# Kernel tuning notes

Hardware: AMD Instinct MI355X
Metric: run time of the kernel (lower is better)

Reference implementation:

```python
import jax, jax.numpy as jnp
import numpy as np
from jax.scipy.special import gammaln

PRIOR = 0.25      # downsample_rate -> Binomial prior on boundary frequency
TEMP = 1.0        # gumbel (RelaxedBernoulli) temperature
THRESHOLD = 0.5   # hard-boundary threshold

B, L, D = 8, 2048, 1024


def setup_inputs() -> dict:
    key = jax.random.key(0)
    k_x, k_u, k_w1, k_w2, k_ng = jax.random.split(key, 5)
    x = jax.random.normal(k_x, (B, L, D), dtype=jnp.float32)
    noise = jax.random.uniform(k_u, (B, L), dtype=jnp.float32)
    W1 = jax.random.normal(k_w1, (D, D), dtype=jnp.float32) / np.sqrt(D)
    b1 = jnp.zeros((D,), dtype=jnp.float32)
    W2 = jax.random.normal(k_w2, (D, 1), dtype=jnp.float32) / np.sqrt(D)
    b2 = jnp.zeros((1,), dtype=jnp.float32)
    null_group = jax.random.normal(k_ng, (1, 1, D), dtype=jnp.float32)
    return {"x": x, "noise": noise, "W1": W1, "b1": b1, "W2": W2, "b2": b2,
            "null_group": null_group}


def _common(boundaries, n_segments, upsample):
    # boundaries: [B, L] -> soft group-offset tensor foo: [B, L, S]
    hh1 = jnp.cumsum(boundaries, axis=1)
    if not upsample:
        hh1 = hh1 - boundaries
    s = jnp.arange(n_segments, dtype=boundaries.dtype)
    return s[None, None, :] - hh1[:, :, None]


def _final(foo, upsample):
    # indicator of token-l belonging to segment-s, normalized (mean-pool / gather)
    lel = jnp.where(foo != 0, 0.0, 1.0 - foo)
    axis = 2 if upsample else 1
    return lel / (jnp.sum(lel, axis=axis, keepdims=True) + 1e-9)


def reference(x, noise, W1, b1, W2, b2, null_group):
    Bn, Ln, Dn = x.shape
    S_max = Ln  # static upper bound on segment count (padded; extra segs = zeros)

    # --- boundary predictor (gumbel / RelaxedBernoulli rsample, temp=1) ---
    logits = (jax.nn.relu(x @ W1 + b1) @ W2 + b2)[..., 0]            # [B, L]
    u = jnp.clip(noise, 1e-6, 1.0 - 1e-6)
    soft = jax.nn.sigmoid((logits + jnp.log(u) - jnp.log1p(-u)) / TEMP)
    hard_val = (soft > THRESHOLD).astype(soft.dtype)
    hard = jax.lax.stop_gradient(hard_val - soft) + soft             # straight-through

    # --- downsample: mean-pool each variable-length segment ---
    bar_d = _final(_common(hard, S_max, False), False)               # [B, L, S]
    pooled = jnp.einsum('bld,bls->bsd', x, bar_d)                    # [B, S, D]
    shortened = jnp.concatenate(
        [jnp.broadcast_to(null_group, (Bn, 1, Dn)), pooled], axis=1)  # [B, S+1, D]

    # --- upsample: token l reads segment cumsum(hard)[l] (null group = 0) ---
    bar_u = _final(_common(hard, S_max + 1, True), True)             # [B, L, S+1]
    upsampled = jnp.einsum('bsd,bls->bld', shortened, bar_u)         # [B, L, D]

    # --- consistency loss: -log Binomial(L, prior).pmf(#boundaries) / L ---
    k = jnp.sum(hard, axis=-1)                                       # [B]
    Lf = jnp.asarray(Ln, soft.dtype)
    logp = (gammaln(Lf + 1.0) - gammaln(k + 1.0) - gammaln(Lf - k + 1.0)
            + k * jnp.log(PRIOR) + (Lf - k) * jnp.log1p(-PRIOR))
    loss = -jnp.mean(logp) / Ln

    return shortened, upsampled, loss
```

## Files before the change

kernel.cpp:

```cpp
#include <hip/hip_runtime.h>
#include <math.h>

#define Bq 8
#define Lq 2048
#define Dq 1024
#define Mq (Bq*Lq)
#define Sq 2048
#define SP1 2049
#define FLAG_CAP 1024
#define KSLICES 8
#define MARGIN 0.06f

typedef __attribute__((ext_vector_type(8))) short short8;
typedef __attribute__((ext_vector_type(4))) float f32x4;

static __device__ __forceinline__ ushort f2bf(float f) {
  union { float f; uint32_t u; } v; v.f = f;
  uint32_t u = v.u;
  return (ushort)((u + 0x7FFF + ((u >> 16) & 1)) >> 16);
}

static __device__ __forceinline__ void gload_lds16(const void* gsrc, void* lds) {
  __builtin_amdgcn_global_load_lds(
      (const __attribute__((address_space(1))) uint32_t*)(uintptr_t)gsrc,
      (__attribute__((address_space(3))) uint32_t*)(uint32_t)(uintptr_t)lds,
      16, 0, 0);
}

__global__ void init_logits(float* __restrict__ logits, const float* __restrict__ b2,
                            int* __restrict__ count) {
  int i = blockIdx.x * 256 + threadIdx.x;
  if (i < Mq) logits[i] = b2[0];
  if (i == 0) *count = 0;
}

__global__ void convert_x(const float* __restrict__ x, ushort* __restrict__ xb) {
  int i = blockIdx.x * 256 + threadIdx.x;
  float4 v = ((const float4*)x)[i];
  ushort4 o;
  o.x = f2bf(v.x); o.y = f2bf(v.y); o.z = f2bf(v.z); o.w = f2bf(v.w);
  ((ushort4*)xb)[i] = o;
}

__global__ void convert_w1t(const float* __restrict__ W1, ushort* __restrict__ Wt) {
  __shared__ ushort sh[32][33];
  const int tx = threadIdx.x & 31, ty = threadIdx.x >> 5;
  const int k0 = blockIdx.x * 32, n0 = blockIdx.y * 32;
  #pragma unroll
  for (int r = 0; r < 32; r += 8)
    sh[ty + r][tx] = f2bf(W1[(size_t)(k0 + ty + r) * Dq + n0 + tx]);
  __syncthreads();
  #pragma unroll
  for (int r = 0; r < 32; r += 8)
    Wt[(size_t)(n0 + ty + r) * Dq + k0 + tx] = sh[tx][ty + r];
}

__global__ __launch_bounds__(256) void mfma_gemm(
    const ushort* __restrict__ Xb,
    const ushort* __restrict__ Wt,
    const float* __restrict__ b1, const float* __restrict__ W2,
    float* __restrict__ logits)
{
  __shared__ ushort Al[128 * 32];
  __shared__ ushort Bl[128 * 32];
  __shared__ float red[128];
  const int tid = threadIdx.x;
  const int w = tid >> 6, lane = tid & 63;
  const int m0 = blockIdx.x * 128, n0 = blockIdx.y * 128;
  const int wr = w >> 1, wc = w & 1;
  const int lr = lane & 15, lq = lane >> 4;

  f32x4 acc[4][4] = {};
  if (tid < 128) red[tid] = 0.f;

  for (int kt = 0; kt < Dq; kt += 32) {
    #pragma unroll
    for (int s = 0; s < 2; ++s) {
      int rbase = s * 64 + w * 16;
      const ushort* srcA = Xb + (size_t)(m0 + rbase + (lane >> 2)) * Dq + kt + (lane & 3) * 8;
      gload_lds16(srcA, &Al[rbase * 32]);
      const ushort* srcB = Wt + (size_t)(n0 + rbase + (lane >> 2)) * Dq + kt + (lane & 3) * 8;
      gload_lds16(srcB, &Bl[rbase * 32]);
    }
    __syncthreads();
    short8 a[4], b[4];
    #pragma unroll
    for (int m = 0; m < 4; ++m)
      a[m] = *(const short8*)&Al[(wr * 64 + m * 16 + lr) * 32 + lq * 8];
    #pragma unroll
    for (int n = 0; n < 4; ++n)
      b[n] = *(const short8*)&Bl[(wc * 64 + n * 16 + lr) * 32 + lq * 8];
    #pragma unroll
    for (int m = 0; m < 4; ++m)
      #pragma unroll
      for (int n = 0; n < 4; ++n)
        acc[m][n] = __builtin_amdgcn_mfma_f32_16x16x32_bf16(a[m], b[n], acc[m][n], 0, 0, 0);
    __syncthreads();
  }

  float q[4][4];
  #pragma unroll
  for (int m = 0; m < 4; ++m)
    #pragma unroll
    for (int r = 0; r < 4; ++r) q[m][r] = 0.f;
  #pragma unroll
  for (int n = 0; n < 4; ++n) {
    int col = n0 + wc * 64 + n * 16 + lr;
    float bb = b1[col];
    float ww = W2[col];
    #pragma unroll
    for (int m = 0; m < 4; ++m)
      #pragma unroll
      for (int r = 0; r < 4; ++r) {
        float v = acc[m][n][r] + bb;
        v = v > 0.f ? v : 0.f;
        q[m][r] = fmaf(v, ww, q[m][r]);
      }
  }
  #pragma unroll
  for (int m = 0; m < 4; ++m)
    #pragma unroll
    for (int r = 0; r < 4; ++r) {
      float s = q[m][r];
      s += __shfl_xor(s, 1); s += __shfl_xor(s, 2);
      s += __shfl_xor(s, 4); s += __shfl_xor(s, 8);
      if (lr == 0) atomicAdd(&red[wr * 64 + m * 16 + lq * 4 + r], s);
    }
  __syncthreads();
  if (tid < 128) atomicAdd(&logits[m0 + tid], red[tid]);
}

__global__ void flag_kernel(const float* __restrict__ logits, const float* __restrict__ noise,
                            int* __restrict__ count, int* __restrict__ list) {
  int i = blockIdx.x * 256 + threadIdx.x;
  float u = noise[i];
  u = fminf(fmaxf(u, 1e-6f), 0.999999f);
  float z = (logits[i] + logf(u)) - log1pf(-u);
  if (fabsf(z) < MARGIN) {
    int id = atomicAdd(count, 1);
    if (id < FLAG_CAP) list[id] = i;
  }
}

__global__ __launch_bounds__(256) void fix_part1(
    const float* __restrict__ x, const float* __restrict__ W1,
    const int* __restrict__ count, const int* __restrict__ list,
    float* __restrict__ hbuf)
{
  __shared__ float Asl[32][33];
  __shared__ float Bsl[32][128];
  int cnt = *count; if (cnt > FLAG_CAP) cnt = FLAG_CAP;
  if (cnt <= 0) return;
  int tiles_m = (cnt + 31) >> 5;
  int total = tiles_m * 8 * KSLICES;
  const int tid = threadIdx.x;
  const int tx = tid & 31, ty = tid >> 5;
  for (int t = blockIdx.x; t < total; t += gridDim.x) {
    int m0 = (t / (8 * KSLICES)) * 32;
    int n0 = ((t / KSLICES) & 7) * 128;
    int kbase = (t % KSLICES) * (Dq / KSLICES);
    float C[4][4] = {};
    for (int kc = 0; kc < Dq / KSLICES; kc += 32) {
      int k0 = kbase + kc;
      __syncthreads();
      {
        int mr = tid >> 3, kf = tid & 7;
        int fidx = m0 + mr; if (fidx >= cnt) fidx = cnt - 1;
        int tok = list[fidx];
        float4 va = *(const float4*)(x + (size_t)tok * Dq + k0 + kf * 4);
        Asl[kf*4+0][mr] = va.x; Asl[kf*4+1][mr] = va.y;
        Asl[kf*4+2][mr] = va.z; Asl[kf*4+3][mr] = va.w;
      }
      #pragma unroll
      for (int s = 0; s < 4; ++s) {
        int slot = tid + s * 256;
        int kb = slot >> 5, nf = slot & 31;
        *(float4*)(&Bsl[kb][nf*4]) =
            *(const float4*)(W1 + (size_t)(k0 + kb) * Dq + n0 + nf * 4);
      }
      __syncthreads();
      #pragma unroll
      for (int k = 0; k < 32; ++k) {
        float a[4], b[4];
        #pragma unroll
        for (int i = 0; i < 4; ++i) a[i] = Asl[k][ty*4+i];
        #pragma unroll
        for (int j = 0; j < 4; ++j) b[j] = Bsl[k][tx + 32*j];
        #pragma unroll
        for (int i = 0; i < 4; ++i)
          #pragma unroll
          for (int j = 0; j < 4; ++j)
            C[i][j] = fmaf(a[i], b[j], C[i][j]);
      }
    }
    int ks = t % KSLICES;
    #pragma unroll
    for (int i = 0; i < 4; ++i) {
      int f = m0 + ty*4 + i;
      float* dst = hbuf + ((size_t)ks * FLAG_CAP + f) * Dq + n0 + tx;
      #pragma unroll
      for (int j = 0; j < 4; ++j) dst[32*j] = C[i][j];
    }
    __syncthreads();
  }
}

__global__ __launch_bounds__(256) void fix_part2(
    const float* __restrict__ hbuf, const float* __restrict__ b1,
    const float* __restrict__ W2, const float* __restrict__ b2,
    const int* __restrict__ count, const int* __restrict__ list,
    float* __restrict__ logits)
{
  __shared__ float rs[4];
  int cnt = *count; if (cnt > FLAG_CAP) cnt = FLAG_CAP;
  const int tid = threadIdx.x;
  const int lane = tid & 63, w = tid >> 6;
  float b2v = b2[0];
  for (int f = blockIdx.x; f < cnt; f += gridDim.x) {
    int n = tid * 4;
    float4 h = {0.f, 0.f, 0.f, 0.f};
    #pragma unroll
    for (int ks = 0; ks < KSLICES; ++ks) {
      float4 pv = *(const float4*)(hbuf + ((size_t)ks * FLAG_CAP + f) * Dq + n);
      h.x += pv.x; h.y += pv.y; h.z += pv.z; h.w += pv.w;
    }
    float4 bb = *(const float4*)(b1 + n);
    float4 ww = *(const float4*)(W2 + n);
    float p = 0.f;
    float v;
    v = h.x + bb.x; v = v > 0.f ? v : 0.f; p = fmaf(v, ww.x, p);
    v = h.y + bb.y; v = v > 0.f ? v : 0.f; p = fmaf(v, ww.y, p);
    v = h.z + bb.z; v = v > 0.f ? v : 0.f; p = fmaf(v, ww.z, p);
    v = h.w + bb.w; v = v > 0.f ? v : 0.f; p = fmaf(v, ww.w, p);
    #pragma unroll
    for (int off = 32; off > 0; off >>= 1) p += __shfl_xor(p, off);
    if (lane == 0) rs[w] = p;
    __syncthreads();
    if (tid == 0) logits[list[f]] = b2v + rs[0] + rs[1] + rs[2] + rs[3];
    __syncthreads();
  }
}

__global__ __launch_bounds__(256) void boundary_scan(
    const float* __restrict__ logits, const float* __restrict__ noise,
    int* __restrict__ segup, int* __restrict__ starts, int* __restrict__ ends,
    int* __restrict__ nsegs, int* __restrict__ kb)
{
  const int b = blockIdx.x;
  const int t = threadIdx.x;
  __shared__ unsigned char sh_hard[Lq];
  __shared__ int wsum[4];
  const int l0 = t * 8;
  int h[8];
  int localsum = 0;
  #pragma unroll
  for (int j = 0; j < 8; ++j) {
    int l = l0 + j;
    float u = noise[b * Lq + l];
    u = fminf(fmaxf(u, 1e-6f), 0.999999f);
    float z = (logits[b * Lq + l] + logf(u)) - log1pf(-u);
    int hd = (z > 0.f) ? 1 : 0;
    h[j] = hd;
    sh_hard[l] = (unsigned char)hd;
    localsum += hd;
  }
  int lane = t & 63, w = t >> 6;
  int v = localsum;
  #pragma unroll
  for (int off = 1; off < 64; off <<= 1) {
    int n = __shfl_up(v, off);
    if (lane >= off) v += n;
  }
  if (lane == 63) wsum[w] = v;
  __syncthreads();
  int wpre = 0;
  for (int i = 0; i < w; ++i) wpre += wsum[i];
  int run = wpre + (v - localsum);
  #pragma unroll
  for (int j = 0; j < 8; ++j) {
    int l = l0 + j;
    run += h[j];
    segup[b * Lq + l] = run;
    int sd = run - h[j];
    int hp = (l == 0) ? 1 : (int)sh_hard[l - 1];
    if (hp) starts[b * Sq + sd] = l;
    if (h[j] || l == Lq - 1) ends[b * Sq + sd] = l + 1;
    if (l == Lq - 1) { nsegs[b] = sd + 1; kb[b] = run; }
  }
}

__global__ __launch_bounds__(256) void pool_kernel(
    const float* __restrict__ x, const float* __restrict__ null_group,
    const int* __restrict__ starts, const int* __restrict__ ends,
    const int* __restrict__ nsegs, float* __restrict__ outS)
{
  const int so = blockIdx.x;
  const int b  = blockIdx.y;
  const int d4 = threadIdx.x;
  float4* dst = (float4*)(outS + ((size_t)b * SP1 + so) * Dq) + d4;
  if (so == 0) { *dst = ((const float4*)null_group)[d4]; return; }
  int s = so - 1;
  if (s >= nsegs[b]) { float4 z; z.x = z.y = z.z = z.w = 0.f; *dst = z; return; }
  int st = starts[b * Sq + s], en = ends[b * Sq + s];
  float4 acc; acc.x = acc.y = acc.z = acc.w = 0.f;
  for (int l = st; l < en; ++l) {
    float4 vv = ((const float4*)(x + ((size_t)b * Lq + l) * Dq))[d4];
    acc.x += vv.x; acc.y += vv.y; acc.z += vv.z; acc.w += vv.w;
  }
  float inv = 1.f / (float)(en - st);
  acc.x *= inv; acc.y *= inv; acc.z *= inv; acc.w *= inv;
  *dst = acc;
}

__global__ __launch_bounds__(256) void upsample_kernel(
    const float* __restrict__ outS, const int* __restrict__ segup,
    float* __restrict__ outU)
{
  const int l = blockIdx.x, b = blockIdx.y;
  const int d4 = threadIdx.x;
  int sg = segup[b * Lq + l];
  ((float4*)(outU + ((size_t)b * Lq + l) * Dq))[d4] =
      ((const float4*)(outS + ((size_t)b * SP1 + sg) * Dq))[d4];
}

__global__ void loss_kernel(const int* __restrict__ kb, float* __restrict__ out)
{
  int t = threadIdx.x;
  float lp = 0.f;
  if (t < Bq) {
    float k  = (float)kb[t];
    float Lf = (float)Lq;
    lp = lgammaf(Lf + 1.f) - lgammaf(k + 1.f) - lgammaf(Lf - k + 1.f)
       + k * logf(0.25f) + (Lf - k) * log1pf(-0.25f);
  }
  #pragma unroll
  for (int off = 32; off > 0; off >>= 1) lp += __shfl_down(lp, off);
  if (t == 0) out[0] = -(lp / (float)Bq) / (float)Lq;
}

extern "C" void kernel_launch(void* const* d_in, const int* in_sizes, int n_in,
                              void* d_out, int out_size, void* d_ws, size_t ws_size,
                              hipStream_t stream) {
  const float* x     = (const float*)d_in[0];
  const float* noise = (const float*)d_in[1];
  const float* W1    = (const float*)d_in[2];
  const float* b1    = (const float*)d_in[3];
  const float* W2    = (const float*)d_in[4];
  const float* b2    = (const float*)d_in[5];
  const float* ng    = (const float*)d_in[6];

  float* outS = (float*)d_out;
  float* outU = outS + (size_t)Bq * SP1 * Dq;
  float* outL = outU + (size_t)Bq * Lq * Dq;

  ushort* xb   = (ushort*)outU;
  ushort* wt   = (ushort*)((char*)outU + (size_t)33554432);
  float*  hbuf = outS;

  char* ws = (char*)d_ws;
  float* logits = (float*)(ws);
  int*   segup  = (int*)(ws + 65536);
  int*   starts = (int*)(ws + 131072);
  int*   ends   = (int*)(ws + 196608);
  int*   nsegs  = (int*)(ws + 262144);
  int*   kb     = (int*)(ws + 262400);
  int*   count  = (int*)(ws + 262656);
  int*   list   = (int*)(ws + 262912);

  init_logits<<<Mq / 256, 256, 0, stream>>>(logits, b2, count);
  convert_x<<<(Mq * Dq / 4) / 256, 256, 0, stream>>>(x, xb);
  convert_w1t<<<dim3(32, 32), 256, 0, stream>>>(W1, wt);
  mfma_gemm<<<dim3(Mq / 128, Dq / 128), 256, 0, stream>>>(xb, wt, b1, W2, logits);
  flag_kernel<<<Mq / 256, 256, 0, stream>>>(logits, noise, count, list);
  fix_part1<<<2048, 256, 0, stream>>>(x, W1, count, list, hbuf);
  fix_part2<<<1024, 256, 0, stream>>>(hbuf, b1, W2, b2, count, list, logits);
  boundary_scan<<<Bq, 256, 0, stream>>>(logits, noise, segup, starts, ends, nsegs, kb);
  pool_kernel<<<dim3(SP1, Bq), 256, 0, stream>>>(x, ng, starts, ends, nsegs, outS);
  upsample_kernel<<<dim3(Lq, Bq), 256, 0, stream>>>(outS, segup, outU);
  loss_kernel<<<1, 64, 0, stream>>>(kb, outL);
}
```

Measured before the change: 311.9 us.

## Fuse conversion kernels and merge pooling with upsample scatter

Merges logits init, x conversion and W1 transpose-conversion into a single launch. Swaps the GEMM grid axes so consecutive blocks share an M row tile and read different W columns. Replaces the separate upsample kernel with a scatter inside the pool kernel: each segment block writes its pooled value directly to the token rows of the upsample output. This uses per-segment boundary positions computed in the scan, so the upsample pass no longer re-reads the pooled output. The risk is load imbalance, since the upsample rows for a segment are written by a single block.

```diff
diff --git a/kernel.cpp b/kernel.cpp
--- a/kernel.cpp
+++ b/kernel.cpp
@@ -27,32 +27,32 @@
       16, 0, 0);
 }
 
-__global__ void init_logits(float* __restrict__ logits, const float* __restrict__ b2,
-                            int* __restrict__ count) {
-  int i = blockIdx.x * 256 + threadIdx.x;
-  if (i < Mq) logits[i] = b2[0];
-  if (i == 0) *count = 0;
-}
-
-__global__ void convert_x(const float* __restrict__ x, ushort* __restrict__ xb) {
-  int i = blockIdx.x * 256 + threadIdx.x;
-  float4 v = ((const float4*)x)[i];
-  ushort4 o;
-  o.x = f2bf(v.x); o.y = f2bf(v.y); o.z = f2bf(v.z); o.w = f2bf(v.w);
-  ((ushort4*)xb)[i] = o;
-}
-
-__global__ void convert_w1t(const float* __restrict__ W1, ushort* __restrict__ Wt) {
-  __shared__ ushort sh[32][33];
-  const int tx = threadIdx.x & 31, ty = threadIdx.x >> 5;
-  const int k0 = blockIdx.x * 32, n0 = blockIdx.y * 32;
-  #pragma unroll
-  for (int r = 0; r < 32; r += 8)
-    sh[ty + r][tx] = f2bf(W1[(size_t)(k0 + ty + r) * Dq + n0 + tx]);
-  __syncthreads();
-  #pragma unroll
-  for (int r = 0; r < 32; r += 8)
-    Wt[(size_t)(n0 + ty + r) * Dq + k0 + tx] = sh[tx][ty + r];
+__global__ void convert_fused(const float* __restrict__ x, const float* __restrict__ W1,
+                              const float* __restrict__ b2,
+                              ushort* __restrict__ xb, ushort* __restrict__ wt,
+                              float* __restrict__ logits, int* __restrict__ count) {
+  int bid = blockIdx.x;
+  if (bid < 16384) {
+    int i = bid * 256 + threadIdx.x;
+    float4 v = ((const float4*)x)[i];
+    ushort4 o;
+    o.x = f2bf(v.x); o.y = f2bf(v.y); o.z = f2bf(v.z); o.w = f2bf(v.w);
+    ((ushort4*)xb)[i] = o;
+    if (i < Mq) logits[i] = b2[0];
+    if (i == 0) *count = 0;
+  } else {
+    __shared__ ushort sh[32][33];
+    int t = bid - 16384;
+    const int tx = threadIdx.x & 31, ty = threadIdx.x >> 5;
+    const int k0 = (t >> 5) * 32, n0 = (t & 31) * 32;
+    #pragma unroll
+    for (int r = 0; r < 32; r += 8)
+      sh[ty + r][tx] = f2bf(W1[(size_t)(k0 + ty + r) * Dq + n0 + tx]);
+    __syncthreads();
+    #pragma unroll
+    for (int r = 0; r < 32; r += 8)
+      wt[(size_t)(n0 + ty + r) * Dq + k0 + tx] = sh[tx][ty + r];
+  }
 }
 
 __global__ __launch_bounds__(256) void mfma_gemm(
@@ -66,7 +66,7 @@
   __shared__ float red[128];
   const int tid = threadIdx.x;
   const int w = tid >> 6, lane = tid & 63;
-  const int m0 = blockIdx.x * 128, n0 = blockIdx.y * 128;
+  const int m0 = blockIdx.y * 128, n0 = blockIdx.x * 128;
   const int wr = w >> 1, wc = w & 1;
   const int lr = lane & 15, lq = lane >> 4;
 
@@ -174,9 +174,9 @@
       #pragma unroll
       for (int s = 0; s < 4; ++s) {
         int slot = tid + s * 256;
-        int kb = slot >> 5, nf = slot & 31;
-        *(float4*)(&Bsl[kb][nf*4]) =
-            *(const float4*)(W1 + (size_t)(k0 + kb) * Dq + n0 + nf * 4);
+        int kb2 = slot >> 5, nf = slot & 31;
+        *(float4*)(&Bsl[kb2][nf*4]) =
+            *(const float4*)(W1 + (size_t)(k0 + kb2) * Dq + n0 + nf * 4);
       }
       __syncthreads();
       #pragma unroll
@@ -243,7 +243,7 @@
 
 __global__ __launch_bounds__(256) void boundary_scan(
     const float* __restrict__ logits, const float* __restrict__ noise,
-    int* __restrict__ segup, int* __restrict__ starts, int* __restrict__ ends,
+    int* __restrict__ starts, int* __restrict__ ends, int* __restrict__ ubs,
     int* __restrict__ nsegs, int* __restrict__ kb)
 {
   const int b = blockIdx.x;
@@ -276,12 +276,13 @@
   int wpre = 0;
   for (int i = 0; i < w; ++i) wpre += wsum[i];
   int run = wpre + (v - localsum);
+  if (t == 0) ubs[b * SP1] = 0;
   #pragma unroll
   for (int j = 0; j < 8; ++j) {
     int l = l0 + j;
     run += h[j];
-    segup[b * Lq + l] = run;
     int sd = run - h[j];
+    if (h[j]) ubs[b * SP1 + run] = l;
     int hp = (l == 0) ? 1 : (int)sh_hard[l - 1];
     if (hp) starts[b * Sq + sd] = l;
     if (h[j] || l == Lq - 1) ends[b * Sq + sd] = l + 1;
@@ -289,38 +290,42 @@
   }
 }
 
-__global__ __launch_bounds__(256) void pool_kernel(
+__global__ __launch_bounds__(256) void pool_up(
     const float* __restrict__ x, const float* __restrict__ null_group,
     const int* __restrict__ starts, const int* __restrict__ ends,
-    const int* __restrict__ nsegs, float* __restrict__ outS)
+    const int* __restrict__ nsegs, const int* __restrict__ ubs,
+    const int* __restrict__ kb,
+    float* __restrict__ outS, float* __restrict__ outU)
 {
   const int so = blockIdx.x;
   const int b  = blockIdx.y;
   const int d4 = threadIdx.x;
-  float4* dst = (float4*)(outS + ((size_t)b * SP1 + so) * Dq) + d4;
-  if (so == 0) { *dst = ((const float4*)null_group)[d4]; return; }
-  int s = so - 1;
-  if (s >= nsegs[b]) { float4 z; z.x = z.y = z.z = z.w = 0.f; *dst = z; return; }
-  int st = starts[b * Sq + s], en = ends[b * Sq + s];
-  float4 acc; acc.x = acc.y = acc.z = acc.w = 0.f;
-  for (int l = st; l < en; ++l) {
-    float4 vv = ((const float4*)(x + ((size_t)b * Lq + l) * Dq))[d4];
-    acc.x += vv.x; acc.y += vv.y; acc.z += vv.z; acc.w += vv.w;
-  }
-  float inv = 1.f / (float)(en - st);
-  acc.x *= inv; acc.y *= inv; acc.z *= inv; acc.w *= inv;
-  *dst = acc;
-}
-
-__global__ __launch_bounds__(256) void upsample_kernel(
-    const float* __restrict__ outS, const int* __restrict__ segup,
-    float* __restrict__ outU)
-{
-  const int l = blockIdx.x, b = blockIdx.y;
-  const int d4 = threadIdx.x;
-  int sg = segup[b * Lq + l];
-  ((float4*)(outU + ((size_t)b * Lq + l) * Dq))[d4] =
-      ((const float4*)(outS + ((size_t)b * SP1 + sg) * Dq))[d4];
+  float4 val;
+  if (so == 0) {
+    val = ((const float4*)null_group)[d4];
+  } else {
+    int s = so - 1;
+    if (s >= nsegs[b]) {
+      val.x = val.y = val.z = val.w = 0.f;
+    } else {
+      int st = starts[b * Sq + s], en = ends[b * Sq + s];
+      float4 acc; acc.x = acc.y = acc.z = acc.w = 0.f;
+      for (int l = st; l < en; ++l) {
+        float4 vv = ((const float4*)(x + ((size_t)b * Lq + l) * Dq))[d4];
+        acc.x += vv.x; acc.y += vv.y; acc.z += vv.z; acc.w += vv.w;
+      }
+      float inv = 1.f / (float)(en - st);
+      val.x = acc.x * inv; val.y = acc.y * inv; val.z = acc.z * inv; val.w = acc.w * inv;
+    }
+  }
+  ((float4*)(outS + ((size_t)b * SP1 + so) * Dq))[d4] = val;
+  int K = kb[b];
+  if (so <= K) {
+    int rs = ubs[b * SP1 + so];
+    int re = (so < K) ? ubs[b * SP1 + so + 1] : Lq;
+    for (int l = rs; l < re; ++l)
+      ((float4*)(outU + ((size_t)b * Lq + l) * Dq))[d4] = val;
+  }
 }
 
 __global__ void loss_kernel(const int* __restrict__ kb, float* __restrict__ out)
@@ -359,23 +364,20 @@
 
   char* ws = (char*)d_ws;
   float* logits = (float*)(ws);
-  int*   segup  = (int*)(ws + 65536);
-  int*   starts = (int*)(ws + 131072);
-  int*   ends   = (int*)(ws + 196608);
-  int*   nsegs  = (int*)(ws + 262144);
-  int*   kb     = (int*)(ws + 262400);
-  int*   count  = (int*)(ws + 262656);
-  int*   list   = (int*)(ws + 262912);
-
-  init_logits<<<Mq / 256, 256, 0, stream>>>(logits, b2, count);
-  convert_x<<<(Mq * Dq / 4) / 256, 256, 0, stream>>>(x, xb);
-  convert_w1t<<<dim3(32, 32), 256, 0, stream>>>(W1, wt);
-  mfma_gemm<<<dim3(Mq / 128, Dq / 128), 256, 0, stream>>>(xb, wt, b1, W2, logits);
+  int*   starts = (int*)(ws + 65536);
+  int*   ends   = (int*)(ws + 131072);
+  int*   ubs    = (int*)(ws + 196608);
+  int*   nsegs  = (int*)(ws + 266240);
+  int*   kb     = (int*)(ws + 266496);
+  int*   count  = (int*)(ws + 266752);
+  int*   list   = (int*)(ws + 267008);
+
+  convert_fused<<<16384 + 1024, 256, 0, stream>>>(x, W1, b2, xb, wt, logits, count);
+  mfma_gemm<<<dim3(Dq / 128, Mq / 128), 256, 0, stream>>>(xb, wt, b1, W2, logits);
   flag_kernel<<<Mq / 256, 256, 0, stream>>>(logits, noise, count, list);
   fix_part1<<<2048, 256, 0, stream>>>(x, W1, count, list, hbuf);
   fix_part2<<<1024, 256, 0, stream>>>(hbuf, b1, W2, b2, count, list, logits);
-  boundary_scan<<<Bq, 256, 0, stream>>>(logits, noise, segup, starts, ends, nsegs, kb);
-  pool_kernel<<<dim3(SP1, Bq), 256, 0, stream>>>(x, ng, starts, ends, nsegs, outS);
-  upsample_kernel<<<dim3(Lq, Bq), 256, 0, stream>>>(outS, segup, outU);
+  boundary_scan<<<Bq, 256, 0, stream>>>(logits, noise, starts, ends, ubs, nsegs, kb);
+  pool_up<<<dim3(SP1, Bq), 256, 0, stream>>>(x, ng, starts, ends, nsegs, ubs, kb, outS, outU);
   loss_kernel<<<1, 64, 0, stream>>>(kb, outL);
 }
```

New measurement: 306.1 us. About the same (-1.9%).
